# Optimization experiments

Measured on AMD Instinct MI355X. Metric: run time of the kernel, lower is better.

The kernel has to match this reference:

```python
import jax, jax.numpy as jnp
import numpy as np

N, H = 1024, 12
SQK, SV, PQK, PV = 16, 16, 4, 8
C1, C2, COUT = 384, 128, 384


def setup_inputs() -> dict:
    key = jax.random.key(0)
    ks = jax.random.split(key, 12)
    inputs_1d = jax.random.normal(ks[0], (N, C1), jnp.float32)
    inputs_2d = jax.random.normal(ks[1], (N, N, C2), jnp.float32)
    mask = jnp.ones((N, 1), jnp.float32)
    # proper-ish rigid frames: orthonormal rotations via batched QR
    rot = jnp.linalg.qr(jax.random.normal(ks[2], (N, 3, 3), jnp.float32))[0]
    trans = jax.random.normal(ks[3], (N, 3), jnp.float32)
    s = 0.02
    params = dict(
        w_q_scalar=jax.random.normal(ks[4], (C1, H * SQK), jnp.float32) * s,
        b_q_scalar=jnp.zeros((H * SQK,), jnp.float32),
        w_kv_scalar=jax.random.normal(ks[5], (C1, H * (SQK + SV)), jnp.float32) * s,
        b_kv_scalar=jnp.zeros((H * (SQK + SV),), jnp.float32),
        w_q_point=jax.random.normal(ks[6], (C1, H * 3 * PQK), jnp.float32) * s,
        b_q_point=jnp.zeros((H * 3 * PQK,), jnp.float32),
        w_kv_point=jax.random.normal(ks[7], (C1, H * 3 * (PQK + PV)), jnp.float32) * s,
        b_kv_point=jnp.zeros((H * 3 * (PQK + PV),), jnp.float32),
        w_2d=jax.random.normal(ks[8], (C2, H), jnp.float32) * s,
        b_2d=jnp.zeros((H,), jnp.float32),
        tpw=jnp.ones((H,), jnp.float32),
        w_out=jax.random.normal(ks[9], (H * (C2 + SV + 4 * PV), COUT), jnp.float32) * s,
        b_out=jnp.zeros((COUT,), jnp.float32),
    )
    return dict(inputs_1d=inputs_1d, inputs_2d=inputs_2d, mask=mask, rot=rot, trans=trans, **params)


def _forward(inputs_1d, inputs_2d, mask, rot, trans,
             w_q_scalar, b_q_scalar, w_kv_scalar, b_kv_scalar,
             w_q_point, b_q_point, w_kv_point, b_kv_point,
             w_2d, b_2d, tpw, w_out, b_out):
    n = inputs_1d.shape[0]
    scalar_w = (1.0 / (3 * SQK)) ** 0.5            # sqrt(1/(3*scalar_variance))
    point_w = (1.0 / (3 * PQK * 4.5)) ** 0.5       # sqrt(1/(3*point_variance))
    w2d_scale = (1.0 / 3.0) ** 0.5

    q_scalar = (inputs_1d @ w_q_scalar + b_q_scalar).reshape(n, H, SQK)
    kv_scalar = (inputs_1d @ w_kv_scalar + b_kv_scalar).reshape(n, H, SQK + SV)
    k_scalar, v_scalar = kv_scalar[..., :SQK], kv_scalar[..., SQK:]

    def to_global(flat, p):
        # flat: [n, 3*H*p] split into x,y,z chunks (matches torch split order)
        pts = jnp.stack(jnp.split(flat, 3, axis=-1), axis=-1)   # [n, H*p, 3]
        g = jnp.einsum('nij,npj->npi', rot, pts) + trans[:, None, :]
        return g.reshape(n, H, p, 3)

    q_pt = to_global(inputs_1d @ w_q_point + b_q_point, PQK)            # [n,H,PQK,3]
    kv_pt = to_global(inputs_1d @ w_kv_point + b_kv_point, PQK + PV)
    k_pt, v_pt = kv_pt[:, :, :PQK], kv_pt[:, :, PQK:]

    pw = jax.nn.softplus(tpw) * point_w                                 # [H]
    qp = q_pt.transpose(1, 0, 2, 3)                                     # [H,n,PQK,3]
    kp = k_pt.transpose(1, 0, 2, 3)
    # -0.5*w_h*sum_p |q-k|^2 expanded as q2+k2-2qk to avoid [H,n,n,PQK,3] temp
    q2 = jnp.sum(qp * qp, axis=(-1, -2))                                # [H,n]
    k2 = jnp.sum(kp * kp, axis=(-1, -2))
    cross = jnp.einsum('hnpc,hmpc->hnm', qp, kp)
    attn_qk_point = -0.5 * pw[:, None, None] * (q2[:, :, None] + k2[:, None, :] - 2.0 * cross)

    attn_qk_scalar = jnp.einsum('hnc,hmc->hnm',
                                scalar_w * q_scalar.transpose(1, 0, 2),
                                k_scalar.transpose(1, 0, 2))
    a2d = (inputs_2d @ w_2d + b_2d).transpose(2, 0, 1)                  # [H,n,n]
    logits = attn_qk_scalar + attn_qk_point + a2d * w2d_scale
    mask_2d = mask * mask.T                                             # [n,n]
    logits = logits - 1e5 * (1.0 - mask_2d)
    attn = jax.nn.softmax(logits, axis=-1)                              # [H,n,n]

    res_scalar = jnp.einsum('hnm,hmc->nhc', attn, v_scalar.transpose(1, 0, 2)).reshape(n, H * SV)
    vp = v_pt.transpose(1, 0, 2, 3)                                     # [H,n,PV,3]
    res_pt_g = jnp.einsum('hnm,hmpc->nhpc', attn, vp).reshape(n, H * PV, 3)
    # invert_point: local = R^T (global - t)
    res_pt_l = jnp.einsum('nji,npj->npi', rot, res_pt_g - trans[:, None, :])
    dist = jnp.sqrt(1e-8 + jnp.sum(res_pt_l * res_pt_l, axis=-1))       # [n, H*PV]
    attn_2d = jnp.einsum('hnm,nmc->nhc', attn, inputs_2d).reshape(n, H * C2)

    final = jnp.concatenate([res_scalar, res_pt_l[..., 0], res_pt_l[..., 1],
                             res_pt_l[..., 2], dist, attn_2d], axis=-1)  # [n, 2112]
    return final @ w_out + b_out


def reference(inputs_1d, inputs_2d, mask, rot, trans,
              w_q_scalar, b_q_scalar, w_kv_scalar, b_kv_scalar,
              w_q_point, b_q_point, w_kv_point, b_kv_point,
              w_2d, b_2d, tpw, w_out, b_out):
    return _forward(inputs_1d, inputs_2d, mask, rot, trans,
                    w_q_scalar, b_q_scalar, w_kv_scalar, b_kv_scalar,
                    w_q_point, b_q_point, w_kv_point, b_kv_point,
                    w_2d, b_2d, tpw, w_out, b_out)
```

## Files before the change

### kernel.cpp

```cpp
#include <hip/hip_runtime.h>
#include <hip/hip_bf16.h>
#include <cstddef>

#define NN 1024
#define HH 12
#define SQK 16
#define SV 16
#define PQK 4
#define PV 8
#define C1 384
#define C2 128
#define COUT 384

#define HSQK (HH*SQK)
#define HKV  (HH*(SQK+SV))
#define QPF  (HH*3*PQK)
#define KVPF (HH*3*(PQK+PV))
#define FDIM (HH*(C2+SV+4*PV))

__device__ __constant__ const float SCALAR_W  = 0.14433756729740643f;
__device__ __constant__ const float POINT_W   = 0.13608276348795434f;
__device__ __constant__ const float W2D_SCALE = 0.5773502691896258f;

constexpr size_t OFF_QS     = 0;
constexpr size_t OFF_KVS    = OFF_QS     + 196608;
constexpr size_t OFF_QPF    = OFF_KVS    + 393216;
constexpr size_t OFF_KVPF   = OFF_QPF    + 147456;
constexpr size_t OFF_QPTG   = OFF_KVPF   + 442368;
constexpr size_t OFF_KVPTG  = OFF_QPTG   + 147456;
constexpr size_t OFF_Q2     = OFF_KVPTG  + 442368;
constexpr size_t OFF_K2     = OFF_Q2     + 12288;
constexpr size_t OFF_PW     = OFF_K2     + 12288;
constexpr size_t OFF_VT     = OFF_PW     + 64;
constexpr size_t OFF_RESPTG = OFF_VT     + 491520;
constexpr size_t OFF_FINAL  = OFF_RESPTG + 294912;
constexpr size_t OFF_LOGITS = OFF_FINAL  + 2162688;

template <bool ATOMIC>
__device__ void gemm_tile_128x64(const float* __restrict__ A, const float* __restrict__ W,
                                 const float* __restrict__ bias, float* __restrict__ C,
                                 int K, int Ncols, int m0, int n0, int k0, int ktiles,
                                 bool addbias)
{
    __shared__ float As[16][136];
    __shared__ float Bs[16][68];
    const int t  = threadIdx.x;
    const int tx = t & 15;
    const int ty = t >> 4;

    float acc[8][4];
#pragma unroll
    for (int i = 0; i < 8; ++i)
#pragma unroll
        for (int j = 0; j < 4; ++j) acc[i][j] = 0.f;

    for (int kt = 0; kt < ktiles; ++kt) {
        const int kb = k0 + kt * 16;
        {
            const int mi = t >> 1, k8 = (t & 1) * 8;
            const float* src = A + (size_t)(m0 + mi) * K + kb + k8;
            float4 v0 = *(const float4*)(src);
            float4 v1 = *(const float4*)(src + 4);
            As[k8 + 0][mi] = v0.x; As[k8 + 1][mi] = v0.y;
            As[k8 + 2][mi] = v0.z; As[k8 + 3][mi] = v0.w;
            As[k8 + 4][mi] = v1.x; As[k8 + 5][mi] = v1.y;
            As[k8 + 6][mi] = v1.z; As[k8 + 7][mi] = v1.w;
        }
        {
            const int kk = t >> 4, n4 = (t & 15) * 4;
            const int col = n0 + n4;
            float4 v = make_float4(0.f, 0.f, 0.f, 0.f);
            if (col < Ncols) v = *(const float4*)(W + (size_t)(kb + kk) * Ncols + col);
            *(float4*)&Bs[kk][n4] = v;
        }
        __syncthreads();
#pragma unroll
        for (int kk = 0; kk < 16; ++kk) {
            float bv[4];
            *(float4*)bv = *(const float4*)&Bs[kk][tx * 4];
            float av[8];
            *(float4*)&av[0] = *(const float4*)&As[kk][ty * 8];
            *(float4*)&av[4] = *(const float4*)&As[kk][ty * 8 + 4];
#pragma unroll
            for (int i = 0; i < 8; ++i)
#pragma unroll
                for (int j = 0; j < 4; ++j) acc[i][j] += av[i] * bv[j];
        }
        __syncthreads();
    }
#pragma unroll
    for (int i = 0; i < 8; ++i) {
        const int row = m0 + ty * 8 + i;
#pragma unroll
        for (int j = 0; j < 4; ++j) {
            const int col = n0 + tx * 4 + j;
            if (col < Ncols) {
                float v = acc[i][j] + (addbias ? bias[col] : 0.f);
                if (ATOMIC) atomicAdd(&C[(size_t)row * Ncols + col], v);
                else        C[(size_t)row * Ncols + col] = v;
            }
        }
    }
}

__global__ __launch_bounds__(256) void proj_kernel(
    const float* __restrict__ A,
    const float* __restrict__ wqs,  const float* __restrict__ bqs,
    const float* __restrict__ wkvs, const float* __restrict__ bkvs,
    const float* __restrict__ wqp,  const float* __restrict__ bqp,
    const float* __restrict__ wkvp, const float* __restrict__ bkvp,
    float* __restrict__ qs, float* __restrict__ kvs,
    float* __restrict__ qpf, float* __restrict__ kvpf)
{
    const int ct = blockIdx.x % 19;
    const int mt = blockIdx.x / 19;
    const float *W, *bias; float* C; int Ncols, n0;
    if (ct < 3)       { W = wqs;  bias = bqs;  C = qs;   Ncols = 192; n0 = ct * 64; }
    else if (ct < 9)  { W = wkvs; bias = bkvs; C = kvs;  Ncols = 384; n0 = (ct - 3) * 64; }
    else if (ct < 12) { W = wqp;  bias = bqp;  C = qpf;  Ncols = 144; n0 = (ct - 9) * 64; }
    else              { W = wkvp; bias = bkvp; C = kvpf; Ncols = 432; n0 = (ct - 12) * 64; }
    gemm_tile_128x64<false>(A, W, bias, C, C1, Ncols, mt * 128, n0, 0, 24, true);
}

__global__ __launch_bounds__(192) void points_kernel(
    const float* __restrict__ qpf, const float* __restrict__ kvpf,
    const float* __restrict__ rot, const float* __restrict__ trans,
    const float* __restrict__ tpw,
    float* __restrict__ qptg, float* __restrict__ kvptg,
    float* __restrict__ q2, float* __restrict__ k2, float* __restrict__ pw)
{
    __shared__ float lq[48 * 3];
    __shared__ float lkv[144 * 3];
    const int n = blockIdx.x, t = threadIdx.x;
    float r[9], tr[3];
#pragma unroll
    for (int i = 0; i < 9; ++i) r[i] = rot[n * 9 + i];
#pragma unroll
    for (int i = 0; i < 3; ++i) tr[i] = trans[n * 3 + i];

    if (t < 48) {
        float p0 = qpf[n * QPF + t], p1 = qpf[n * QPF + 48 + t], p2 = qpf[n * QPF + 96 + t];
#pragma unroll
        for (int i = 0; i < 3; ++i)
            lq[t * 3 + i] = r[i * 3 + 0] * p0 + r[i * 3 + 1] * p1 + r[i * 3 + 2] * p2 + tr[i];
    }
    if (t < 144) {
        float p0 = kvpf[(size_t)n * KVPF + t];
        float p1 = kvpf[(size_t)n * KVPF + 144 + t];
        float p2 = kvpf[(size_t)n * KVPF + 288 + t];
#pragma unroll
        for (int i = 0; i < 3; ++i)
            lkv[t * 3 + i] = r[i * 3 + 0] * p0 + r[i * 3 + 1] * p1 + r[i * 3 + 2] * p2 + tr[i];
    }
    __syncthreads();
    if (t < 48) {
#pragma unroll
        for (int i = 0; i < 3; ++i) qptg[(size_t)n * QPF + t * 3 + i] = lq[t * 3 + i];
    }
    if (t < 144) {
#pragma unroll
        for (int i = 0; i < 3; ++i) kvptg[(size_t)n * KVPF + t * 3 + i] = lkv[t * 3 + i];
    }
    if (t < HH) {
        float s = 0.f;
#pragma unroll
        for (int p = 0; p < 4; ++p)
#pragma unroll
            for (int i = 0; i < 3; ++i) { float v = lq[(t * 4 + p) * 3 + i]; s += v * v; }
        q2[t * NN + n] = s;
        float s2 = 0.f;
#pragma unroll
        for (int p = 0; p < 4; ++p)
#pragma unroll
            for (int i = 0; i < 3; ++i) { float v = lkv[(t * 12 + p) * 3 + i]; s2 += v * v; }
        k2[t * NN + n] = s2;
        if (n == 0) {
            float x = tpw[t];
            float sp = (x > 20.f) ? x : log1pf(__expf(x));
            pw[t] = sp * POINT_W;
        }
    }
}

__global__ __launch_bounds__(256) void vt_kernel(const float* __restrict__ kvs,
                                                 const float* __restrict__ kvptg,
                                                 float* __restrict__ vT)
{
    const int idx = blockIdx.x * 256 + threadIdx.x;
    const int r = idx >> 10, m = idx & 1023;
    float val;
    if (r < 192) {
        const int h = r >> 4, c = r & 15;
        val = kvs[(size_t)m * HKV + h * 32 + 16 + c];
    } else {
        const int q = r - 192;
        const int h = q / 24, rem = q % 24;
        val = kvptg[(size_t)m * KVPF + h * 36 + 12 + rem];
    }
    vT[(size_t)r * NN + m] = val;
}

__global__ __launch_bounds__(256) void logits_kernel(
    const float* __restrict__ in2d, const float* __restrict__ w2d, const float* __restrict__ b2d,
    const float* __restrict__ qs, const float* __restrict__ kvs,
    const float* __restrict__ qptg, const float* __restrict__ kvptg,
    const float* __restrict__ q2, const float* __restrict__ k2,
    const float* __restrict__ pw, const float* __restrict__ mask,
    float* __restrict__ logits)
{
    __shared__ float w2s[C2 * HH];
    const int t = threadIdx.x;
    for (int i = t; i < C2 * HH; i += 256) w2s[i] = w2d[i];
    __syncthreads();

    const int n = blockIdx.x >> 2;
    const int m = ((blockIdx.x & 3) << 8) + t;

    const float4* row = (const float4*)(in2d + ((size_t)n * NN + m) * C2);
    float a2[HH];
#pragma unroll
    for (int h = 0; h < HH; ++h) a2[h] = 0.f;
    for (int c4 = 0; c4 < C2 / 4; ++c4) {
        float4 v = row[c4];
        const float* w = &w2s[c4 * 4 * HH];
#pragma unroll
        for (int h = 0; h < HH; ++h)
            a2[h] += v.x * w[h] + v.y * w[HH + h] + v.z * w[2 * HH + h] + v.w * w[3 * HH + h];
    }
    const float mval = -100000.f * (1.f - mask[n] * mask[m]);
    const float* qbase = qs + (size_t)n * HSQK;
    const float* kbase = kvs + (size_t)m * HKV;
    const float* qpb = qptg + (size_t)n * QPF;
    const float* kpb = kvptg + (size_t)m * KVPF;

    for (int h = 0; h < HH; ++h) {
        const float4* qq = (const float4*)(qbase + h * SQK);
        const float4* kq = (const float4*)(kbase + h * (SQK + SV));
        float sd = 0.f;
#pragma unroll
        for (int j = 0; j < 4; ++j) {
            float4 a = qq[j], b = kq[j];
            sd += a.x * b.x + a.y * b.y + a.z * b.z + a.w * b.w;
        }
        const float4* qp = (const float4*)(qpb + h * 3 * PQK);
        const float4* kp = (const float4*)(kpb + h * 3 * (PQK + PV));
        float cr = 0.f;
#pragma unroll
        for (int j = 0; j < 3; ++j) {
            float4 a = qp[j], b = kp[j];
            cr += a.x * b.x + a.y * b.y + a.z * b.z + a.w * b.w;
        }
        float pt = -0.5f * pw[h] * (q2[h * NN + n] + k2[h * NN + m] - 2.f * cr);
        float lg = SCALAR_W * sd + pt + W2D_SCALE * (a2[h] + b2d[h]) + mval;
        logits[((size_t)h * NN + n) * NN + m] = lg;
    }
}

__global__ __launch_bounds__(256) void softmax_kernel(float* __restrict__ logits)
{
    const size_t rowid = blockIdx.x;
    float* p = logits + rowid * NN;
    const int t = threadIdx.x;
    float4 v = ((float4*)p)[t];
    float mx = fmaxf(fmaxf(v.x, v.y), fmaxf(v.z, v.w));
#pragma unroll
    for (int o = 32; o; o >>= 1) mx = fmaxf(mx, __shfl_xor(mx, o));
    __shared__ float redm[4];
    __shared__ float reds[4];
    const int w = t >> 6, lane = t & 63;
    if (lane == 0) redm[w] = mx;
    __syncthreads();
    mx = fmaxf(fmaxf(redm[0], redm[1]), fmaxf(redm[2], redm[3]));
    float e0 = __expf(v.x - mx), e1 = __expf(v.y - mx), e2 = __expf(v.z - mx), e3 = __expf(v.w - mx);
    float s = e0 + e1 + e2 + e3;
#pragma unroll
    for (int o = 32; o; o >>= 1) s += __shfl_xor(s, o);
    if (lane == 0) reds[w] = s;
    __syncthreads();
    s = reds[0] + reds[1] + reds[2] + reds[3];
    const float inv = 1.f / s;
    ((float4*)p)[t] = make_float4(e0 * inv, e1 * inv, e2 * inv, e3 * inv);
}

__global__ __launch_bounds__(256) void attn2d_kernel(
    const float* __restrict__ attn, const float* __restrict__ in2d, float* __restrict__ fin)
{
    __shared__ float la[NN * HH];
    const int t = threadIdx.x;
    const int n = blockIdx.x;
#pragma unroll
    for (int h = 0; h < HH; ++h)
#pragma unroll
        for (int k = 0; k < 4; ++k) {
            const int m = t + (k << 8);
            la[m * HH + h] = attn[((size_t)h * NN + n) * NN + m];
        }
    __syncthreads();

    const int c0 = t & 31;
    const int ml = t >> 5;
    float acc[HH][4];
#pragma unroll
    for (int h = 0; h < HH; ++h)
#pragma unroll
        for (int j = 0; j < 4; ++j) acc[h][j] = 0.f;

    const float* base = in2d + (size_t)n * NN * C2;
    for (int m = ml; m < NN; m += 8) {
        const float* r2 = base + (size_t)m * C2;
        float v0 = r2[c0], v1 = r2[c0 + 32], v2 = r2[c0 + 64], v3 = r2[c0 + 96];
        const float* am = &la[m * HH];
        float av[HH];
        *(float4*)&av[0] = *(const float4*)(am);
        *(float4*)&av[4] = *(const float4*)(am + 4);
        *(float4*)&av[8] = *(const float4*)(am + 8);
#pragma unroll
        for (int h = 0; h < HH; ++h) {
            acc[h][0] += av[h] * v0; acc[h][1] += av[h] * v1;
            acc[h][2] += av[h] * v2; acc[h][3] += av[h] * v3;
        }
    }
    for (int h = 0; h < HH; ++h) {
        __syncthreads();
        la[(ml << 7) + c0]      = acc[h][0];
        la[(ml << 7) + c0 + 32] = acc[h][1];
        la[(ml << 7) + c0 + 64] = acc[h][2];
        la[(ml << 7) + c0 + 96] = acc[h][3];
        __syncthreads();
        if (t < 128) {
            float s = 0.f;
#pragma unroll
            for (int l = 0; l < 8; ++l) s += la[(l << 7) + t];
            fin[(size_t)n * FDIM + 576 + (h << 7) + t] = s;
        }
    }
}

__global__ __launch_bounds__(256) void attnv_kernel(
    const float* __restrict__ attn, const float* __restrict__ vT,
    float* __restrict__ fin, float* __restrict__ resptg)
{
    __shared__ float la[HH * 1040];
    const int t = threadIdx.x;
    const int n = blockIdx.x;
#pragma unroll
    for (int h = 0; h < HH; ++h)
#pragma unroll
        for (int k = 0; k < 4; ++k) {
            const int m = t + (k << 8);
            la[h * 1040 + m] = attn[((size_t)h * NN + n) * NN + m];
        }
    __syncthreads();
    for (int r = t; r < 480; r += 256) {
        const int h = (r < 192) ? (r >> 4) : ((r - 192) / 24);
        const float4* vr = (const float4*)(vT + (size_t)r * NN);
        const float4* ar = (const float4*)&la[h * 1040];
        float s = 0.f;
        for (int q = 0; q < NN / 4; ++q) {
            float4 a = ar[q], v = vr[q];
            s += a.x * v.x + a.y * v.y + a.z * v.z + a.w * v.w;
        }
        if (r < 192) fin[(size_t)n * FDIM + r] = s;
        else         resptg[(size_t)n * 288 + (r - 192)] = s;
    }
}

__global__ __launch_bounds__(128) void ptout_kernel(
    const float* __restrict__ resptg, const float* __restrict__ rot,
    const float* __restrict__ trans, float* __restrict__ fin)
{
    const int n = blockIdx.x, t = threadIdx.x;
    if (t >= 96) return;
    float g0 = resptg[(size_t)n * 288 + t * 3 + 0];
    float g1 = resptg[(size_t)n * 288 + t * 3 + 1];
    float g2 = resptg[(size_t)n * 288 + t * 3 + 2];
    float d0 = g0 - trans[n * 3 + 0];
    float d1 = g1 - trans[n * 3 + 1];
    float d2 = g2 - trans[n * 3 + 2];
    float l0 = rot[n * 9 + 0] * d0 + rot[n * 9 + 3] * d1 + rot[n * 9 + 6] * d2;
    float l1 = rot[n * 9 + 1] * d0 + rot[n * 9 + 4] * d1 + rot[n * 9 + 7] * d2;
    float l2 = rot[n * 9 + 2] * d0 + rot[n * 9 + 5] * d1 + rot[n * 9 + 8] * d2;
    const size_t base = (size_t)n * FDIM;
    fin[base + 192 + t] = l0;
    fin[base + 288 + t] = l1;
    fin[base + 384 + t] = l2;
    fin[base + 480 + t] = sqrtf(1e-8f + l0 * l0 + l1 * l1 + l2 * l2);
}

__global__ __launch_bounds__(256) void outgemm_kernel(
    const float* __restrict__ fin, const float* __restrict__ wout,
    const float* __restrict__ bout, float* __restrict__ out)
{
    const int n0 = blockIdx.x * 64;
    const int m0 = blockIdx.y * 128;
    const int z  = blockIdx.z;
    gemm_tile_128x64<true>(fin, wout, bout, out, FDIM, COUT, m0, n0, z * 352, 22, z == 0);
}

extern "C" void kernel_launch(void* const* d_in, const int* in_sizes, int n_in,
                              void* d_out, int out_size, void* d_ws, size_t ws_size,
                              hipStream_t stream)
{
    const float* in1d  = (const float*)d_in[0];
    const float* in2d  = (const float*)d_in[1];
    const float* mask  = (const float*)d_in[2];
    const float* rot   = (const float*)d_in[3];
    const float* trans = (const float*)d_in[4];
    const float* wqs   = (const float*)d_in[5];
    const float* bqs   = (const float*)d_in[6];
    const float* wkvs  = (const float*)d_in[7];
    const float* bkvs  = (const float*)d_in[8];
    const float* wqp   = (const float*)d_in[9];
    const float* bqp   = (const float*)d_in[10];
    const float* bkvpW = (const float*)d_in[11];
    const float* bkvpB = (const float*)d_in[12];
    const float* w2d   = (const float*)d_in[13];
    const float* b2d   = (const float*)d_in[14];
    const float* tpw   = (const float*)d_in[15];
    const float* wout  = (const float*)d_in[16];
    const float* bout  = (const float*)d_in[17];

    float* ws     = (float*)d_ws;
    float* qs     = ws + OFF_QS;
    float* kvs    = ws + OFF_KVS;
    float* qpf    = ws + OFF_QPF;
    float* kvpf   = ws + OFF_KVPF;
    float* qptg   = ws + OFF_QPTG;
    float* kvptg  = ws + OFF_KVPTG;
    float* q2     = ws + OFF_Q2;
    float* k2     = ws + OFF_K2;
    float* pw     = ws + OFF_PW;
    float* vT     = ws + OFF_VT;
    float* resptg = ws + OFF_RESPTG;
    float* fin    = ws + OFF_FINAL;
    float* logits = ws + OFF_LOGITS;

    hipMemsetAsync(d_out, 0, (size_t)out_size * sizeof(float), stream);

    proj_kernel<<<152, 256, 0, stream>>>(in1d, wqs, bqs, wkvs, bkvs, wqp, bqp, bkvpW, bkvpB,
                                         qs, kvs, qpf, kvpf);
    points_kernel<<<NN, 192, 0, stream>>>(qpf, kvpf, rot, trans, tpw, qptg, kvptg, q2, k2, pw);
    vt_kernel<<<1920, 256, 0, stream>>>(kvs, kvptg, vT);
    logits_kernel<<<4096, 256, 0, stream>>>(in2d, w2d, b2d, qs, kvs, qptg, kvptg,
                                            q2, k2, pw, mask, logits);
    softmax_kernel<<<HH * NN, 256, 0, stream>>>(logits);
    attn2d_kernel<<<NN, 256, 0, stream>>>(logits, in2d, fin);
    attnv_kernel<<<NN, 256, 0, stream>>>(logits, vT, fin, resptg);
    ptout_kernel<<<NN, 128, 0, stream>>>(resptg, rot, trans, fin);
    outgemm_kernel<<<dim3(6, 8, 6), 256, 0, stream>>>(fin, wout, bout, (float*)d_out);
}
```

Before: 1.423 ms.

## Split logits into tiled 2D-bias kernel and register-tiled QK GEMM kernel

```diff
diff --git a/kernel.cpp b/kernel.cpp
--- a/kernel.cpp
+++ b/kernel.cpp
@@ -200,59 +200,155 @@
     vT[(size_t)r * NN + m] = val;
 }
 
-__global__ __launch_bounds__(256) void logits_kernel(
-    const float* __restrict__ in2d, const float* __restrict__ w2d, const float* __restrict__ b2d,
+__global__ __launch_bounds__(256) void a2d_kernel(
+    const float* __restrict__ in2d, const float* __restrict__ w2d,
+    const float* __restrict__ b2d, const float* __restrict__ mask,
+    float* __restrict__ logits)
+{
+    __shared__ float As[128 * 65];
+    __shared__ float w2s[C2 * HH];
+    __shared__ float red[4][64][13];
+    const int t  = threadIdx.x;
+    const int n  = blockIdx.y;
+    const int m0 = blockIdx.x * 64;
+
+    for (int i = t; i < C2 * HH; i += 256) w2s[i] = w2d[i];
+
+    const int rl = t & 7;
+    const int c4 = t >> 3;
+    const float* base = in2d + ((size_t)n * NN + m0) * C2;
+    float4 v[8];
+#pragma unroll
+    for (int it = 0; it < 8; ++it)
+        v[it] = *(const float4*)(base + (size_t)(it * 8 + rl) * C2 + c4 * 4);
+#pragma unroll
+    for (int it = 0; it < 8; ++it) {
+        const int r = it * 8 + rl;
+        As[(c4 * 4 + 0) * 65 + r] = v[it].x;
+        As[(c4 * 4 + 1) * 65 + r] = v[it].y;
+        As[(c4 * 4 + 2) * 65 + r] = v[it].z;
+        As[(c4 * 4 + 3) * 65 + r] = v[it].w;
+    }
+    __syncthreads();
+
+    {
+        const int r  = t & 63;
+        const int cq = t >> 6;
+        float acc[HH];
+#pragma unroll
+        for (int h = 0; h < HH; ++h) acc[h] = 0.f;
+        const int cbeg = cq * 32;
+#pragma unroll 8
+        for (int ci = 0; ci < 32; ++ci) {
+            const int c = cbeg + ci;
+            const float a = As[c * 65 + r];
+            const float* w = &w2s[c * HH];
+#pragma unroll
+            for (int h = 0; h < HH; ++h) acc[h] += a * w[h];
+        }
+#pragma unroll
+        for (int h = 0; h < HH; ++h) red[cq][r][h] = acc[h];
+    }
+    __syncthreads();
+
+    {
+        const int r2 = t & 63;
+        const int hb = (t >> 6) * 3;
+        const float mval = -100000.f * (1.f - mask[n] * mask[m0 + r2]);
+#pragma unroll
+        for (int j = 0; j < 3; ++j) {
+            const int h = hb + j;
+            const float s = red[0][r2][h] + red[1][r2][h] + red[2][r2][h] + red[3][r2][h];
+            logits[((size_t)h * NN + n) * NN + m0 + r2] = W2D_SCALE * (s + b2d[h]) + mval;
+        }
+    }
+}
+
+__global__ __launch_bounds__(256) void qk_kernel(
     const float* __restrict__ qs, const float* __restrict__ kvs,
     const float* __restrict__ qptg, const float* __restrict__ kvptg,
     const float* __restrict__ q2, const float* __restrict__ k2,
-    const float* __restrict__ pw, const float* __restrict__ mask,
-    float* __restrict__ logits)
-{
-    __shared__ float w2s[C2 * HH];
-    const int t = threadIdx.x;
-    for (int i = t; i < C2 * HH; i += 256) w2s[i] = w2d[i];
-    __syncthreads();
-
-    const int n = blockIdx.x >> 2;
-    const int m = ((blockIdx.x & 3) << 8) + t;
-
-    const float4* row = (const float4*)(in2d + ((size_t)n * NN + m) * C2);
-    float a2[HH];
-#pragma unroll
-    for (int h = 0; h < HH; ++h) a2[h] = 0.f;
-    for (int c4 = 0; c4 < C2 / 4; ++c4) {
-        float4 v = row[c4];
-        const float* w = &w2s[c4 * 4 * HH];
-#pragma unroll
-        for (int h = 0; h < HH; ++h)
-            a2[h] += v.x * w[h] + v.y * w[HH + h] + v.z * w[2 * HH + h] + v.w * w[3 * HH + h];
-    }
-    const float mval = -100000.f * (1.f - mask[n] * mask[m]);
-    const float* qbase = qs + (size_t)n * HSQK;
-    const float* kbase = kvs + (size_t)m * HKV;
-    const float* qpb = qptg + (size_t)n * QPF;
-    const float* kpb = kvptg + (size_t)m * KVPF;
-
-    for (int h = 0; h < HH; ++h) {
-        const float4* qq = (const float4*)(qbase + h * SQK);
-        const float4* kq = (const float4*)(kbase + h * (SQK + SV));
-        float sd = 0.f;
-#pragma unroll
-        for (int j = 0; j < 4; ++j) {
-            float4 a = qq[j], b = kq[j];
-            sd += a.x * b.x + a.y * b.y + a.z * b.z + a.w * b.w;
-        }
-        const float4* qp = (const float4*)(qpb + h * 3 * PQK);
-        const float4* kp = (const float4*)(kpb + h * 3 * (PQK + PV));
-        float cr = 0.f;
-#pragma unroll
-        for (int j = 0; j < 3; ++j) {
-            float4 a = qp[j], b = kp[j];
-            cr += a.x * b.x + a.y * b.y + a.z * b.z + a.w * b.w;
-        }
-        float pt = -0.5f * pw[h] * (q2[h * NN + n] + k2[h * NN + m] - 2.f * cr);
-        float lg = SCALAR_W * sd + pt + W2D_SCALE * (a2[h] + b2d[h]) + mval;
-        logits[((size_t)h * NN + n) * NN + m] = lg;
+    const float* __restrict__ pw, float* __restrict__ logits)
+{
+    __shared__ float qT[30][132];
+    __shared__ float kT[30][132];
+    const int t  = threadIdx.x;
+    const int h  = blockIdx.x;
+    const int n0 = blockIdx.y * 128;
+    const int m0 = blockIdx.z * 128;
+    const float pwh = pw[h];
+
+    for (int i = t; i < 512; i += 256) {
+        const int nl = i >> 2, cq = i & 3;
+        float4 a = *(const float4*)(qs + (size_t)(n0 + nl) * HSQK + h * SQK + cq * 4);
+        qT[4 * cq + 0][nl] = SCALAR_W * a.x;
+        qT[4 * cq + 1][nl] = SCALAR_W * a.y;
+        qT[4 * cq + 2][nl] = SCALAR_W * a.z;
+        qT[4 * cq + 3][nl] = SCALAR_W * a.w;
+    }
+    for (int i = t; i < 384; i += 256) {
+        const int nl = i / 3, c3 = i - nl * 3;
+        float4 a = *(const float4*)(qptg + (size_t)(n0 + nl) * QPF + h * 3 * PQK + c3 * 4);
+        qT[16 + 4 * c3 + 0][nl] = pwh * a.x;
+        qT[16 + 4 * c3 + 1][nl] = pwh * a.y;
+        qT[16 + 4 * c3 + 2][nl] = pwh * a.z;
+        qT[16 + 4 * c3 + 3][nl] = pwh * a.w;
+    }
+    if (t < 128) {
+        qT[28][t] = -0.5f * pwh * q2[(size_t)h * NN + n0 + t];
+        qT[29][t] = 1.f;
+    }
+    for (int i = t; i < 512; i += 256) {
+        const int ml = i >> 2, cq = i & 3;
+        float4 a = *(const float4*)(kvs + (size_t)(m0 + ml) * HKV + h * (SQK + SV) + cq * 4);
+        kT[4 * cq + 0][ml] = a.x;
+        kT[4 * cq + 1][ml] = a.y;
+        kT[4 * cq + 2][ml] = a.z;
+        kT[4 * cq + 3][ml] = a.w;
+    }
+    for (int i = t; i < 384; i += 256) {
+        const int ml = i / 3, c3 = i - ml * 3;
+        float4 a = *(const float4*)(kvptg + (size_t)(m0 + ml) * KVPF + h * 3 * (PQK + PV) + c3 * 4);
+        kT[16 + 4 * c3 + 0][ml] = a.x;
+        kT[16 + 4 * c3 + 1][ml] = a.y;
+        kT[16 + 4 * c3 + 2][ml] = a.z;
+        kT[16 + 4 * c3 + 3][ml] = a.w;
+    }
+    if (t < 128) {
+        kT[28][t] = 1.f;
+        kT[29][t] = -0.5f * pwh * k2[(size_t)h * NN + m0 + t];
+    }
+    __syncthreads();
+
+    const int tn = t >> 4;
+    const int tm = t & 15;
+    float acc[8][8];
+#pragma unroll
+    for (int i = 0; i < 8; ++i)
+#pragma unroll
+        for (int j = 0; j < 8; ++j) acc[i][j] = 0.f;
+
+    for (int c = 0; c < 30; ++c) {
+        float qv[8], kv[8];
+        *(float4*)&qv[0] = *(const float4*)&qT[c][tn * 8];
+        *(float4*)&qv[4] = *(const float4*)&qT[c][tn * 8 + 4];
+        *(float4*)&kv[0] = *(const float4*)&kT[c][tm * 4];
+        *(float4*)&kv[4] = *(const float4*)&kT[c][64 + tm * 4];
+#pragma unroll
+        for (int i = 0; i < 8; ++i)
+#pragma unroll
+            for (int j = 0; j < 8; ++j) acc[i][j] += qv[i] * kv[j];
+    }
+
+#pragma unroll
+    for (int i = 0; i < 8; ++i) {
+        float* lg = logits + ((size_t)h * NN + n0 + tn * 8 + i) * NN + m0;
+        float4* p0 = (float4*)(lg + tm * 4);
+        float4* p1 = (float4*)(lg + 64 + tm * 4);
+        float4 a = *p0, b = *p1;
+        a.x += acc[i][0]; a.y += acc[i][1]; a.z += acc[i][2]; a.w += acc[i][3];
+        b.x += acc[i][4]; b.y += acc[i][5]; b.z += acc[i][6]; b.w += acc[i][7];
+        *p0 = a; *p1 = b;
     }
 }
 
@@ -441,8 +537,8 @@
                                          qs, kvs, qpf, kvpf);
     points_kernel<<<NN, 192, 0, stream>>>(qpf, kvpf, rot, trans, tpw, qptg, kvptg, q2, k2, pw);
     vt_kernel<<<1920, 256, 0, stream>>>(kvs, kvptg, vT);
-    logits_kernel<<<4096, 256, 0, stream>>>(in2d, w2d, b2d, qs, kvs, qptg, kvptg,
-                                            q2, k2, pw, mask, logits);
+    a2d_kernel<<<dim3(16, NN), 256, 0, stream>>>(in2d, w2d, b2d, mask, logits);
+    qk_kernel<<<dim3(HH, 8, 8), 256, 0, stream>>>(qs, kvs, qptg, kvptg, q2, k2, pw, logits);
     softmax_kernel<<<HH * NN, 256, 0, stream>>>(logits);
     attn2d_kernel<<<NN, 256, 0, stream>>>(logits, in2d, fin);
     attnv_kernel<<<NN, 256, 0, stream>>>(logits, vT, fin, resptg);
```

Result: faster. 1.301 ms (-8.6%).

## Fuse logits, online softmax and attn-2d aggregation into one per-row kernel

Applied to the files above, without the earlier changes.

```diff
diff --git a/kernel.cpp b/kernel.cpp
--- a/kernel.cpp
+++ b/kernel.cpp
@@ -35,6 +35,7 @@
 constexpr size_t OFF_RESPTG = OFF_VT     + 491520;
 constexpr size_t OFF_FINAL  = OFF_RESPTG + 294912;
 constexpr size_t OFF_LOGITS = OFF_FINAL  + 2162688;
+constexpr size_t OFF_KTAB   = OFF_LOGITS + 12582912;
 
 template <bool ATOMIC>
 __device__ void gemm_tile_128x64(const float* __restrict__ A, const float* __restrict__ W,
@@ -200,168 +201,221 @@
     vT[(size_t)r * NN + m] = val;
 }
 
-__global__ __launch_bounds__(256) void logits_kernel(
-    const float* __restrict__ in2d, const float* __restrict__ w2d, const float* __restrict__ b2d,
-    const float* __restrict__ qs, const float* __restrict__ kvs,
-    const float* __restrict__ qptg, const float* __restrict__ kvptg,
-    const float* __restrict__ q2, const float* __restrict__ k2,
-    const float* __restrict__ pw, const float* __restrict__ mask,
-    float* __restrict__ logits)
-{
-    __shared__ float w2s[C2 * HH];
-    const int t = threadIdx.x;
-    for (int i = t; i < C2 * HH; i += 256) w2s[i] = w2d[i];
+__global__ __launch_bounds__(256) void tab_kernel(
+    const float* __restrict__ kvs, const float* __restrict__ kvptg,
+    const float* __restrict__ k2, const float* __restrict__ pw,
+    float* __restrict__ ktab)
+{
+    const int id = blockIdx.x * 256 + threadIdx.x;
+    const int h = id >> 10, m = id & 1023;
+    float v[32];
+    const float4* ks = (const float4*)(kvs + (size_t)m * HKV + h * 32);
+#pragma unroll
+    for (int j = 0; j < 4; ++j) *(float4*)&v[j * 4] = ks[j];
+    const float4* kp = (const float4*)(kvptg + (size_t)m * KVPF + h * 36);
+#pragma unroll
+    for (int j = 0; j < 3; ++j) *(float4*)&v[16 + j * 4] = kp[j];
+    v[28] = 1.f;
+    v[29] = -0.5f * pw[h] * k2[(size_t)h * NN + m];
+    v[30] = 1.f;
+    v[31] = 0.f;
+    float4* dst = (float4*)(ktab + (size_t)id * 32);
+#pragma unroll
+    for (int j = 0; j < 8; ++j) dst[j] = *(const float4*)&v[j * 4];
+}
+
+__global__ __launch_bounds__(512) void fused_kernel(
+    const float* __restrict__ in2d, const float* __restrict__ w2d,
+    const float* __restrict__ b2d, const float* __restrict__ mask,
+    const float* __restrict__ qs, const float* __restrict__ qptg,
+    const float* __restrict__ q2, const float* __restrict__ pw,
+    const float* __restrict__ ktab,
+    float* __restrict__ attn, float* __restrict__ fin)
+{
+    __shared__ __align__(16) float pL[12 * 1024];
+    __shared__ float xsT[128 * 33];
+    __shared__ __align__(16) float w2sT[12 * 128];
+    __shared__ __align__(16) float qt[12 * 32];
+    __shared__ float pe[12 * 32];
+    __shared__ float maskc[32];
+    __shared__ float st_m[12], st_s[12], resc[12];
+
+    const int n = blockIdx.x, t = threadIdx.x;
+
+    for (int i = t; i < 1536; i += 512) {
+        const int h = i >> 7, c = i & 127;
+        w2sT[i] = W2D_SCALE * w2d[c * HH + h];
+    }
+    if (t < 384) {
+        const int h = t >> 5, j = t & 31;
+        float v;
+        if (j < 16)       v = SCALAR_W * qs[(size_t)n * HSQK + h * 16 + j];
+        else if (j < 28)  v = pw[h] * qptg[(size_t)n * QPF + h * 12 + (j - 16)];
+        else if (j == 28) v = -0.5f * pw[h] * q2[(size_t)h * NN + n];
+        else if (j == 29) v = 1.f;
+        else if (j == 30) v = W2D_SCALE * b2d[h];
+        else              v = 0.f;
+        qt[t] = v;
+    }
+    if (t < 12) { st_m[t] = -3.0e38f; st_s[t] = 0.f; resc[t] = 0.f; }
+    const float maskn = mask[n];
+    const int hx = t >> 7, cx = t & 127;
+    float xa0 = 0.f, xa1 = 0.f, xa2 = 0.f;
     __syncthreads();
 
-    const int n = blockIdx.x >> 2;
-    const int m = ((blockIdx.x & 3) << 8) + t;
-
-    const float4* row = (const float4*)(in2d + ((size_t)n * NN + m) * C2);
-    float a2[HH];
-#pragma unroll
-    for (int h = 0; h < HH; ++h) a2[h] = 0.f;
-    for (int c4 = 0; c4 < C2 / 4; ++c4) {
-        float4 v = row[c4];
-        const float* w = &w2s[c4 * 4 * HH];
-#pragma unroll
-        for (int h = 0; h < HH; ++h)
-            a2[h] += v.x * w[h] + v.y * w[HH + h] + v.z * w[2 * HH + h] + v.w * w[3 * HH + h];
-    }
-    const float mval = -100000.f * (1.f - mask[n] * mask[m]);
-    const float* qbase = qs + (size_t)n * HSQK;
-    const float* kbase = kvs + (size_t)m * HKV;
-    const float* qpb = qptg + (size_t)n * QPF;
-    const float* kpb = kvptg + (size_t)m * KVPF;
-
-    for (int h = 0; h < HH; ++h) {
-        const float4* qq = (const float4*)(qbase + h * SQK);
-        const float4* kq = (const float4*)(kbase + h * (SQK + SV));
-        float sd = 0.f;
-#pragma unroll
-        for (int j = 0; j < 4; ++j) {
-            float4 a = qq[j], b = kq[j];
-            sd += a.x * b.x + a.y * b.y + a.z * b.z + a.w * b.w;
-        }
-        const float4* qp = (const float4*)(qpb + h * 3 * PQK);
-        const float4* kp = (const float4*)(kpb + h * 3 * (PQK + PV));
-        float cr = 0.f;
-#pragma unroll
-        for (int j = 0; j < 3; ++j) {
-            float4 a = qp[j], b = kp[j];
-            cr += a.x * b.x + a.y * b.y + a.z * b.z + a.w * b.w;
-        }
-        float pt = -0.5f * pw[h] * (q2[h * NN + n] + k2[h * NN + m] - 2.f * cr);
-        float lg = SCALAR_W * sd + pt + W2D_SCALE * (a2[h] + b2d[h]) + mval;
-        logits[((size_t)h * NN + n) * NN + m] = lg;
-    }
-}
-
-__global__ __launch_bounds__(256) void softmax_kernel(float* __restrict__ logits)
-{
-    const size_t rowid = blockIdx.x;
-    float* p = logits + rowid * NN;
-    const int t = threadIdx.x;
-    float4 v = ((float4*)p)[t];
-    float mx = fmaxf(fmaxf(v.x, v.y), fmaxf(v.z, v.w));
-#pragma unroll
-    for (int o = 32; o; o >>= 1) mx = fmaxf(mx, __shfl_xor(mx, o));
-    __shared__ float redm[4];
-    __shared__ float reds[4];
-    const int w = t >> 6, lane = t & 63;
-    if (lane == 0) redm[w] = mx;
-    __syncthreads();
-    mx = fmaxf(fmaxf(redm[0], redm[1]), fmaxf(redm[2], redm[3]));
-    float e0 = __expf(v.x - mx), e1 = __expf(v.y - mx), e2 = __expf(v.z - mx), e3 = __expf(v.w - mx);
-    float s = e0 + e1 + e2 + e3;
-#pragma unroll
-    for (int o = 32; o; o >>= 1) s += __shfl_xor(s, o);
-    if (lane == 0) reds[w] = s;
-    __syncthreads();
-    s = reds[0] + reds[1] + reds[2] + reds[3];
-    const float inv = 1.f / s;
-    ((float4*)p)[t] = make_float4(e0 * inv, e1 * inv, e2 * inv, e3 * inv);
-}
-
-__global__ __launch_bounds__(256) void attn2d_kernel(
-    const float* __restrict__ attn, const float* __restrict__ in2d, float* __restrict__ fin)
-{
-    __shared__ float la[NN * HH];
-    const int t = threadIdx.x;
-    const int n = blockIdx.x;
-#pragma unroll
-    for (int h = 0; h < HH; ++h)
-#pragma unroll
-        for (int k = 0; k < 4; ++k) {
-            const int m = t + (k << 8);
-            la[m * HH + h] = attn[((size_t)h * NN + n) * NN + m];
-        }
-    __syncthreads();
-
-    const int c0 = t & 31;
-    const int ml = t >> 5;
-    float acc[HH][4];
-#pragma unroll
-    for (int h = 0; h < HH; ++h)
-#pragma unroll
-        for (int j = 0; j < 4; ++j) acc[h][j] = 0.f;
-
-    const float* base = in2d + (size_t)n * NN * C2;
-    for (int m = ml; m < NN; m += 8) {
-        const float* r2 = base + (size_t)m * C2;
-        float v0 = r2[c0], v1 = r2[c0 + 32], v2 = r2[c0 + 64], v3 = r2[c0 + 96];
-        const float* am = &la[m * HH];
-        float av[HH];
-        *(float4*)&av[0] = *(const float4*)(am);
-        *(float4*)&av[4] = *(const float4*)(am + 4);
-        *(float4*)&av[8] = *(const float4*)(am + 8);
-#pragma unroll
-        for (int h = 0; h < HH; ++h) {
-            acc[h][0] += av[h] * v0; acc[h][1] += av[h] * v1;
-            acc[h][2] += av[h] * v2; acc[h][3] += av[h] * v3;
-        }
-    }
-    for (int h = 0; h < HH; ++h) {
-        __syncthreads();
-        la[(ml << 7) + c0]      = acc[h][0];
-        la[(ml << 7) + c0 + 32] = acc[h][1];
-        la[(ml << 7) + c0 + 64] = acc[h][2];
-        la[(ml << 7) + c0 + 96] = acc[h][3];
-        __syncthreads();
-        if (t < 128) {
-            float s = 0.f;
-#pragma unroll
-            for (int l = 0; l < 8; ++l) s += la[(l << 7) + t];
-            fin[(size_t)n * FDIM + 576 + (h << 7) + t] = s;
-        }
-    }
-}
-
-__global__ __launch_bounds__(256) void attnv_kernel(
+    for (int mc = 0; mc < 32; ++mc) {
+        const int m0 = mc * 32;
+        const float* src = in2d + ((size_t)n * NN + m0) * C2;
+#pragma unroll
+        for (int k2_ = 0; k2_ < 2; ++k2_) {
+            const int f = t + (k2_ << 9);
+            const int row = f >> 5, c4 = f & 31;
+            float4 v = *(const float4*)(src + (size_t)row * C2 + c4 * 4);
+            xsT[(c4 * 4 + 0) * 33 + row] = v.x;
+            xsT[(c4 * 4 + 1) * 33 + row] = v.y;
+            xsT[(c4 * 4 + 2) * 33 + row] = v.z;
+            xsT[(c4 * 4 + 3) * 33 + row] = v.w;
+        }
+        if (t < 32) maskc[t] = mask[m0 + t];
+        __syncthreads();
+
+        if (t < 384) {
+            const int h = t >> 5, mloc = t & 31, m = m0 + mloc;
+            float p0 = 0.f, p1 = 0.f, p2 = 0.f, p3 = 0.f;
+            const float* wh = &w2sT[h * 128];
+            const float* xc = &xsT[mloc];
+#pragma unroll 8
+            for (int c4 = 0; c4 < 32; ++c4) {
+                float4 w = *(const float4*)(wh + c4 * 4);
+                p0 += w.x * xc[(c4 * 4 + 0) * 33];
+                p1 += w.y * xc[(c4 * 4 + 1) * 33];
+                p2 += w.z * xc[(c4 * 4 + 2) * 33];
+                p3 += w.w * xc[(c4 * 4 + 3) * 33];
+            }
+            const float a2d = (p0 + p1) + (p2 + p3);
+            const float4* kt4 = (const float4*)(ktab + ((size_t)h * NN + m) * 32);
+            const float4* qh  = (const float4*)&qt[h * 32];
+            float qk0 = 0.f, qk1 = 0.f;
+#pragma unroll
+            for (int j = 0; j < 8; j += 2) {
+                float4 a = qh[j],     b = kt4[j];
+                float4 a2_ = qh[j+1], b2_ = kt4[j+1];
+                qk0 += a.x * b.x + a.y * b.y + a.z * b.z + a.w * b.w;
+                qk1 += a2_.x * b2_.x + a2_.y * b2_.y + a2_.z * b2_.z + a2_.w * b2_.w;
+            }
+            const float mval = -100000.f * (1.f - maskn * maskc[mloc]);
+            const float l = (qk0 + qk1) + a2d + mval;
+            pL[h * 1024 + m] = l;
+            float cm = l;
+#pragma unroll
+            for (int off = 16; off; off >>= 1) cm = fmaxf(cm, __shfl_xor(cm, off));
+            const float mOld = st_m[h];
+            const float mNew = fmaxf(mOld, cm);
+            const float pv = __expf(l - mNew);
+            pe[h * 32 + mloc] = pv;
+            float cs = pv;
+#pragma unroll
+            for (int off = 16; off; off >>= 1) cs += __shfl_xor(cs, off);
+            if (mloc == 0) {
+                const float r = __expf(mOld - mNew);
+                st_s[h] = st_s[h] * r + cs;
+                st_m[h] = mNew;
+                resc[h] = r;
+            }
+        }
+        __syncthreads();
+
+        {
+            xa0 *= resc[hx];
+            xa1 *= resc[hx + 4];
+            xa2 *= resc[hx + 8];
+            const float* xv = &xsT[cx * 33];
+            const float* pA = &pe[hx * 32];
+            const float* pB = &pe[(hx + 4) * 32];
+            const float* pC = &pe[(hx + 8) * 32];
+#pragma unroll 8
+            for (int mm = 0; mm < 32; ++mm) {
+                const float x_ = xv[mm];
+                xa0 += pA[mm] * x_;
+                xa1 += pB[mm] * x_;
+                xa2 += pC[mm] * x_;
+            }
+        }
+        __syncthreads();
+    }
+
+#pragma unroll
+    for (int rep = 0; rep < 6; ++rep) {
+        const int task = t + (rep << 9);
+        const int h = task >> 8, q4 = task & 255;
+        const float M = st_m[h], invS = 1.f / st_s[h];
+        float4 l4 = *(const float4*)&pL[h * 1024 + q4 * 4];
+        float4 o;
+        o.x = __expf(l4.x - M) * invS;
+        o.y = __expf(l4.y - M) * invS;
+        o.z = __expf(l4.z - M) * invS;
+        o.w = __expf(l4.w - M) * invS;
+        *(float4*)(attn + ((size_t)h * NN + n) * NN + q4 * 4) = o;
+    }
+    const size_t fb = (size_t)n * FDIM + 576;
+    fin[fb + (size_t)hx * 128 + cx]        = xa0 / st_s[hx];
+    fin[fb + (size_t)(hx + 4) * 128 + cx]  = xa1 / st_s[hx + 4];
+    fin[fb + (size_t)(hx + 8) * 128 + cx]  = xa2 / st_s[hx + 8];
+}
+
+__global__ __launch_bounds__(256) void attnv2_kernel(
     const float* __restrict__ attn, const float* __restrict__ vT,
     float* __restrict__ fin, float* __restrict__ resptg)
 {
-    __shared__ float la[HH * 1040];
+    __shared__ float As2[64 * 68];
+    __shared__ float Vs[40 * 68];
+    const int h = blockIdx.x, n0 = blockIdx.y * 64;
     const int t = threadIdx.x;
-    const int n = blockIdx.x;
-#pragma unroll
-    for (int h = 0; h < HH; ++h)
+    const int tn = t >> 3, tc = t & 7;
+    float acc[2][5];
+#pragma unroll
+    for (int i = 0; i < 2; ++i)
+#pragma unroll
+        for (int j = 0; j < 5; ++j) acc[i][j] = 0.f;
+
+    for (int mc = 0; mc < 16; ++mc) {
+        const int m0 = mc * 64;
 #pragma unroll
         for (int k = 0; k < 4; ++k) {
-            const int m = t + (k << 8);
-            la[h * 1040 + m] = attn[((size_t)h * NN + n) * NN + m];
-        }
-    __syncthreads();
-    for (int r = t; r < 480; r += 256) {
-        const int h = (r < 192) ? (r >> 4) : ((r - 192) / 24);
-        const float4* vr = (const float4*)(vT + (size_t)r * NN);
-        const float4* ar = (const float4*)&la[h * 1040];
-        float s = 0.f;
-        for (int q = 0; q < NN / 4; ++q) {
-            float4 a = ar[q], v = vr[q];
-            s += a.x * v.x + a.y * v.y + a.z * v.z + a.w * v.w;
-        }
-        if (r < 192) fin[(size_t)n * FDIM + r] = s;
-        else         resptg[(size_t)n * 288 + (r - 192)] = s;
+            const int f = t + (k << 8);
+            const int row = f >> 4, q = f & 15;
+            *(float4*)&As2[row * 68 + q * 4] =
+                *(const float4*)(attn + ((size_t)h * NN + n0 + row) * NN + m0 + q * 4);
+        }
+        for (int f = t; f < 640; f += 256) {
+            const int row = f >> 4, q = f & 15;
+            const int rg = (row < 16) ? (h * 16 + row) : (192 + h * 24 + (row - 16));
+            *(float4*)&Vs[row * 68 + q * 4] =
+                *(const float4*)(vT + (size_t)rg * NN + m0 + q * 4);
+        }
+        __syncthreads();
+#pragma unroll
+        for (int q = 0; q < 16; ++q) {
+            float4 a0 = *(const float4*)&As2[(tn * 2 + 0) * 68 + q * 4];
+            float4 a1 = *(const float4*)&As2[(tn * 2 + 1) * 68 + q * 4];
+#pragma unroll
+            for (int j = 0; j < 5; ++j) {
+                float4 vv = *(const float4*)&Vs[(tc * 5 + j) * 68 + q * 4];
+                acc[0][j] += a0.x * vv.x + a0.y * vv.y + a0.z * vv.z + a0.w * vv.w;
+                acc[1][j] += a1.x * vv.x + a1.y * vv.y + a1.z * vv.z + a1.w * vv.w;
+            }
+        }
+        __syncthreads();
+    }
+#pragma unroll
+    for (int i = 0; i < 2; ++i) {
+        const int nn_ = n0 + tn * 2 + i;
+#pragma unroll
+        for (int j = 0; j < 5; ++j) {
+            const int c = tc * 5 + j;
+            if (c < 16) fin[(size_t)nn_ * FDIM + h * 16 + c] = acc[i][j];
+            else        resptg[(size_t)nn_ * 288 + h * 24 + (c - 16)] = acc[i][j];
+        }
     }
 }
 
@@ -433,7 +487,8 @@
     float* vT     = ws + OFF_VT;
     float* resptg = ws + OFF_RESPTG;
     float* fin    = ws + OFF_FINAL;
-    float* logits = ws + OFF_LOGITS;
+    float* attn   = ws + OFF_LOGITS;
+    float* ktab   = ws + OFF_KTAB;
 
     hipMemsetAsync(d_out, 0, (size_t)out_size * sizeof(float), stream);
 
@@ -441,11 +496,10 @@
                                          qs, kvs, qpf, kvpf);
     points_kernel<<<NN, 192, 0, stream>>>(qpf, kvpf, rot, trans, tpw, qptg, kvptg, q2, k2, pw);
     vt_kernel<<<1920, 256, 0, stream>>>(kvs, kvptg, vT);
-    logits_kernel<<<4096, 256, 0, stream>>>(in2d, w2d, b2d, qs, kvs, qptg, kvptg,
-                                            q2, k2, pw, mask, logits);
-    softmax_kernel<<<HH * NN, 256, 0, stream>>>(logits);
-    attn2d_kernel<<<NN, 256, 0, stream>>>(logits, in2d, fin);
-    attnv_kernel<<<NN, 256, 0, stream>>>(logits, vT, fin, resptg);
+    tab_kernel<<<48, 256, 0, stream>>>(kvs, kvptg, k2, pw, ktab);
+    fused_kernel<<<NN, 512, 0, stream>>>(in2d, w2d, b2d, mask, qs, qptg, q2, pw,
+                                         ktab, attn, fin);
+    attnv2_kernel<<<dim3(HH, 16), 256, 0, stream>>>(attn, vT, fin, resptg);
     ptout_kernel<<<NN, 128, 0, stream>>>(resptg, rot, trans, fin);
     outgemm_kernel<<<dim3(6, 8, 6), 256, 0, stream>>>(fin, wout, bout, (float*)d_out);
 }
```

Measured after the change: 1.186 ms. -16.6%, faster.
